# Kernel tuning notes

Hardware: AMD Instinct MI355X
Metric: run time of the kernel (lower is better)

Reference implementation:

```python
import jax, jax.numpy as jnp
import numpy as np

N_MEL = 80


def _bce_with_logits(x, t):
    # mean over all elements, numerically stable
    return jnp.mean(jnp.maximum(x, 0.0) - x * t + jnp.log1p(jnp.exp(-jnp.abs(x))))


def _spectral_mel_loss(pred, target):
    w = np.ones(N_MEL, dtype=np.float32)
    w[N_MEL // 4: 3 * N_MEL // 4] *= 1.5
    w[3 * N_MEL // 4:] *= 0.8
    w = jnp.asarray(w)[None, :, None]
    weighted_mse = jnp.mean((pred * w - target * w) ** 2)
    l1 = jnp.mean(jnp.abs(pred - target))
    dp = pred[:, :, 1:] - pred[:, :, :-1]
    dt = target[:, :, 1:] - target[:, :, :-1]
    spectral = jnp.mean((dp - dt) ** 2)
    return weighted_mse + 0.3 * l1 + 0.2 * spectral


def _perceptual_loss(pred, target):
    fw = jnp.exp(-jnp.arange(N_MEL, dtype=jnp.float32) / 20.0)[None, :, None]
    weighted = ((pred - target) ** 2) * fw
    l1 = jnp.mean(jnp.abs(pred - target))
    return jnp.mean(weighted) + 0.5 * l1


def _style_loss(pred, target):
    mean_loss = jnp.mean((jnp.mean(pred, axis=2) - jnp.mean(target, axis=2)) ** 2)
    # torch.var defaults to unbiased (ddof=1)
    var_loss = jnp.mean((jnp.var(pred, axis=2, ddof=1) - jnp.var(target, axis=2, ddof=1)) ** 2)
    c, t = pred.shape[1], pred.shape[2]
    gram_p = jnp.einsum('bct,bdt->bcd', pred, pred) / (c * t)
    gram_t = jnp.einsum('bct,bdt->bcd', target, target) / (c * t)
    gram_loss = jnp.mean((gram_p - gram_t) ** 2)
    return mean_loss + var_loss + 0.5 * gram_loss


def _monotonic_loss(att):
    # att: [B, mel_len, text_len]; vectorized form of the per-step violation loop
    b, mel_len, _ = att.shape
    peaks = jnp.argmax(att, axis=2).astype(jnp.float32)  # [B, mel_len]
    viol = jnp.maximum(peaks[:, :-1] - peaks[:, 1:], 0.0)
    return jnp.sum(viol) / (b * mel_len)


def setup_inputs() -> dict:
    key = jax.random.key(0)
    ks = jax.random.split(key, 6)
    B, C, T, L = 64, N_MEL, 2000, 200
    return {
        'mel_out': jax.random.normal(ks[0], (B, C, T), jnp.float32),
        'mel_out_postnet': jax.random.normal(ks[1], (B, C, T), jnp.float32),
        'mel_target': jax.random.normal(ks[2], (B, C, T), jnp.float32),
        'gate_out': jax.random.normal(ks[3], (B, T), jnp.float32),
        'gate_target': jax.random.uniform(ks[4], (B, T), jnp.float32),
        'attention_weights': jax.random.uniform(ks[5], (B, T, L), jnp.float32),
    }


def reference(mel_out, mel_out_postnet, mel_target, gate_out, gate_target, attention_weights):
    # loss weights (hparams defaults); guide_loss omitted (method truncated in source)
    mel_w, gate_w, spec_w, perc_w, style_w, mono_w = 1.0, 1.0, 0.3, 0.2, 0.1, 0.1
    gate_inner_w = 1.3  # AdaptiveGateLoss initial_weight

    mel_loss = jnp.mean((mel_out - mel_target) ** 2) + jnp.mean((mel_out_postnet - mel_target) ** 2)
    gate_loss = gate_inner_w * _bce_with_logits(gate_out.reshape(-1, 1), gate_target.reshape(-1, 1))
    spectral = _spectral_mel_loss(mel_out_postnet, mel_target)
    perceptual = _perceptual_loss(mel_out_postnet, mel_target)
    style = _style_loss(mel_out_postnet, mel_target)
    mono = _monotonic_loss(attention_weights)

    total = (mel_w * mel_loss + gate_w * gate_loss + spec_w * spectral
             + perc_w * perceptual + style_w * style + mono_w * mono)
    return total
```

## Files before the change

kernel.cpp:

```cpp
#include <hip/hip_runtime.h>
#include <math.h>

#define N_MEL 80
#define B_    64
#define T_    2000
#define L_    200
#define ROWS   (B_*N_MEL)
#define NTOT   (B_*N_MEL*T_)
#define GATE_N (B_*T_)
#define ATT_ROWS (B_*T_)
#define AV_ROWS 64
#define NVIOL  (ATT_ROWS/AV_ROWS)

#define G_ARGV   NVIOL
#define G_GATE   64
#define G_MELROW ROWS

#define WS_ROWPART 0
#define WS_M8      (WS_ROWPART + ROWS*8)
#define WS_GATEP   (WS_M8 + 8*64*6400)
#define WS_VIOLP   (WS_GATEP + 64)
#define WS_GFP     (WS_VIOLP + NVIOL)

typedef __attribute__((ext_vector_type(8)))  short bf16x8;
typedef __attribute__((ext_vector_type(16))) float f32x16;
typedef unsigned short ush;

__device__ __forceinline__ float blockReduceSum256(float v) {
    __shared__ float red[4];
    #pragma unroll
    for (int off = 32; off; off >>= 1) v += __shfl_down(v, off, 64);
    int lane = threadIdx.x & 63, w = threadIdx.x >> 6;
    if (lane == 0) red[w] = v;
    __syncthreads();
    if (threadIdx.x == 0) v = red[0] + red[1] + red[2] + red[3];
    return v;
}

__device__ __forceinline__ unsigned short f2bf(float f) {
    unsigned u = __float_as_uint(f);
    u = (u + 0x7fffu + ((u >> 16) & 1u)) >> 16;
    return (unsigned short)u;
}

__device__ __forceinline__ void scan_sub(const float* __restrict__ rowp, int q,
                                         float& bOut, int& pOut) {
    const float4* rp = (const float4*)rowp;
    float bx=-1.f, by=-1.f, bz=-1.f, bw=-1.f;
    int jx=0, jy=0, jz=0, jw=0;
    const int n = (q < 2) ? 13 : 12;
    #pragma unroll
    for (int i = 0; i < 13; i++) {
        if (i < n) {
            int j = q + 4*i;
            float4 v = rp[j];
            if (v.x > bx) { bx = v.x; jx = j; }
            if (v.y > by) { by = v.y; jy = j; }
            if (v.z > bz) { bz = v.z; jz = j; }
            if (v.w > bw) { bw = v.w; jw = j; }
        }
    }
    float b = bx; int p = 4*jx;
    if (by > b || (by == b && 4*jy+1 < p)) { b = by; p = 4*jy+1; }
    if (bz > b || (bz == b && 4*jz+2 < p)) { b = bz; p = 4*jz+2; }
    if (bw > b || (bw == b && 4*jw+3 < p)) { b = bw; p = 4*jw+3; }
    bOut = b; pOut = p;
}

__device__ __forceinline__ void merge4(float& b, int& p) {
    #pragma unroll
    for (int m = 1; m <= 2; m <<= 1) {
        float ob = __shfl_xor(b, m, 64);
        int   op = __shfl_xor(p, m, 64);
        if (ob > b || (ob == b && op < p)) { b = ob; p = op; }
    }
}

__global__ __launch_bounds__(256) void k_stream(const float* __restrict__ mo,
                                                const float* __restrict__ mp,
                                                const float* __restrict__ mt,
                                                const float* __restrict__ gx,
                                                const float* __restrict__ gt,
                                                const float* __restrict__ att,
                                                float* __restrict__ ws) {
    const int bid = blockIdx.x;
    float* rowpart = ws + WS_ROWPART;
    float* gatep   = ws + WS_GATEP;
    float* violp   = ws + WS_VIOLP;

    if (bid < G_ARGV) {
        __shared__ float pk[AV_ROWS + 1];
        const int ab = bid;
        const int g = threadIdx.x >> 2;
        const int q = threadIdx.x & 3;
        const int r0 = ab * AV_ROWS;
        const int r  = r0 + g;

        float b; int p;
        scan_sub(att + (long)r * L_, q, b, p);
        merge4(b, p);
        if (q == 0) pk[g] = (float)p;

        const int rb = r0 + AV_ROWS;
        const bool need_b = ((rb % T_) != 0) && (rb < ATT_ROWS);
        if (g == 0 && need_b) {
            float b2; int p2;
            scan_sub(att + (long)rb * L_, q, b2, p2);
            merge4(b2, p2);
            if (q == 0) pk[AV_ROWS] = (float)p2;
        }
        __syncthreads();

        float s = 0;
        if (threadIdx.x < AV_ROWS) {
            int rr = r0 + threadIdx.x;
            if (((rr + 1) % T_) != 0)
                s = fmaxf(pk[threadIdx.x] - pk[threadIdx.x + 1], 0.0f);
        }
        float tot = blockReduceSum256(s);
        if (threadIdx.x == 0) violp[ab] = tot;
        return;
    }

    if (bid < G_ARGV + G_GATE) {
        const int gb = bid - G_ARGV;
        const float4* x4 = (const float4*)gx;
        const float4* t4 = (const float4*)gt;
        float s = 0;
        for (int i = gb*256 + threadIdx.x; i < GATE_N/4; i += G_GATE*256) {
            float4 x = x4[i], t = t4[i];
            float xs[4] = {x.x, x.y, x.z, x.w}, ts[4] = {t.x, t.y, t.z, t.w};
            #pragma unroll
            for (int k = 0; k < 4; k++)
                s += fmaxf(xs[k], 0.0f) - xs[k]*ts[k] + log1pf(expf(-fabsf(xs[k])));
        }
        float tot = blockReduceSum256(s);
        if (threadIdx.x == 0) gatep[gb] = tot;
        return;
    }

    {
        const int row = bid - (G_ARGV + G_GATE);
        const long base = (long)row * T_;
        const float4* mo4 = (const float4*)(mo + base);
        const float4* mp4 = (const float4*)(mp + base);
        const float4* mt4 = (const float4*)(mt + base);

        float s1 = 0, s2 = 0, sl1 = 0, std_ = 0, sp = 0, sp2 = 0, st = 0, st2 = 0;
        for (int i = threadIdx.x; i < T_/4; i += 256) {
            float4 a = mo4[i], p = mp4[i], t = mt4[i];
            float e0 = a.x - t.x, e1 = a.y - t.y, e2 = a.z - t.z, e3 = a.w - t.w;
            s1 += e0*e0 + e1*e1 + e2*e2 + e3*e3;
            float d0 = p.x - t.x, d1 = p.y - t.y, d2 = p.z - t.z, d3 = p.w - t.w;
            s2 += d0*d0 + d1*d1 + d2*d2 + d3*d3;
            sl1 += fabsf(d0) + fabsf(d1) + fabsf(d2) + fabsf(d3);
            sp  += p.x + p.y + p.z + p.w;
            sp2 += p.x*p.x + p.y*p.y + p.z*p.z + p.w*p.w;
            st  += t.x + t.y + t.z + t.w;
            st2 += t.x*t.x + t.y*t.y + t.z*t.z + t.w*t.w;
            float q1 = d1 - d0, q2 = d2 - d1, q3 = d3 - d2;
            std_ += q1*q1 + q2*q2 + q3*q3;
            if (i > 0) {
                float dprev = mp[base + 4*i - 1] - mt[base + 4*i - 1];
                float q0 = d0 - dprev;
                std_ += q0*q0;
            }
        }

        __shared__ float red8[4][8];
        float vals[8] = {s1, s2, sl1, std_, sp, sp2, st, st2};
        #pragma unroll
        for (int k = 0; k < 8; k++) {
            float v = vals[k];
            #pragma unroll
            for (int off = 32; off; off >>= 1) v += __shfl_down(v, off, 64);
            vals[k] = v;
        }
        int lane = threadIdx.x & 63, w = threadIdx.x >> 6;
        if (lane == 0) {
            #pragma unroll
            for (int k = 0; k < 8; k++) red8[w][k] = vals[k];
        }
        __syncthreads();
        if (threadIdx.x == 0) {
            #pragma unroll
            for (int k = 0; k < 8; k++)
                rowpart[row*8 + k] = red8[0][k] + red8[1][k] + red8[2][k] + red8[3][k];
        }
    }
}

__global__ __launch_bounds__(192) void k_gram(const float* __restrict__ mp,
                                              const float* __restrict__ mt,
                                              float* __restrict__ M8) {
    const int b  = blockIdx.x >> 3;
    const int kc = blockIdx.x & 7;
    const int k0 = kc * 256;
    const int NS = (kc < 7) ? 16 : 13;

    __shared__ ush Dls[2][96][24];
    __shared__ ush Sls[2][96][24];

    const int tid  = threadIdx.x;
    const int row  = tid >> 1;
    const int half = tid & 1;
    const int lane = tid & 63;
    const int wv   = tid >> 6;
    const long bbase = (long)b * (N_MEL * T_);
    const float* prow = mp + bbase + (long)row * T_ + k0 + half * 8;
    const float* trow = mt + bbase + (long)row * T_ + k0 + half * 8;
    const bool rv = (row < N_MEL);

    f32x16 acc0 = {}, acc1 = {}, acc2 = {};
    float4 pa0, pa1, ta0, ta1;

    auto loadreg = [&](int s) {
        if (rv) {
            pa0 = *(const float4*)(prow + s*16);
            pa1 = *(const float4*)(prow + s*16 + 4);
            ta0 = *(const float4*)(trow + s*16);
            ta1 = *(const float4*)(trow + s*16 + 4);
        } else {
            pa0 = pa1 = ta0 = ta1 = make_float4(0.f, 0.f, 0.f, 0.f);
        }
    };
    auto writelds = [&](int buf) {
        bf16x8 d, s;
        d[0]=f2bf(pa0.x-ta0.x); d[1]=f2bf(pa0.y-ta0.y); d[2]=f2bf(pa0.z-ta0.z); d[3]=f2bf(pa0.w-ta0.w);
        d[4]=f2bf(pa1.x-ta1.x); d[5]=f2bf(pa1.y-ta1.y); d[6]=f2bf(pa1.z-ta1.z); d[7]=f2bf(pa1.w-ta1.w);
        s[0]=f2bf(pa0.x+ta0.x); s[1]=f2bf(pa0.y+ta0.y); s[2]=f2bf(pa0.z+ta0.z); s[3]=f2bf(pa0.w+ta0.w);
        s[4]=f2bf(pa1.x+ta1.x); s[5]=f2bf(pa1.y+ta1.y); s[6]=f2bf(pa1.z+ta1.z); s[7]=f2bf(pa1.w+ta1.w);
        *(bf16x8*)&Dls[buf][row][half*8] = d;
        *(bf16x8*)&Sls[buf][row][half*8] = s;
    };

    loadreg(0);
    writelds(0);
    __syncthreads();

    const int frow = lane & 31;
    const int fkh  = lane >> 5;
    for (int s = 0; s < NS; s++) {
        const int cur = s & 1;
        if (s + 1 < NS) loadreg(s + 1);
        bf16x8 af = *(const bf16x8*)&Dls[cur][wv*32 + frow][fkh*8];
        bf16x8 b0 = *(const bf16x8*)&Sls[cur][      frow][fkh*8];
        bf16x8 b1 = *(const bf16x8*)&Sls[cur][ 32 + frow][fkh*8];
        bf16x8 b2 = *(const bf16x8*)&Sls[cur][ 64 + frow][fkh*8];
        acc0 = __builtin_amdgcn_mfma_f32_32x32x16_bf16(af, b0, acc0, 0, 0, 0);
        acc1 = __builtin_amdgcn_mfma_f32_32x32x16_bf16(af, b1, acc1, 0, 0, 0);
        acc2 = __builtin_amdgcn_mfma_f32_32x32x16_bf16(af, b2, acc2, 0, 0, 0);
        if (s + 1 < NS) writelds((s + 1) & 1);
        __syncthreads();
    }

    float* Mb = M8 + ((long)(kc * B_ + b)) * 6400;
    #pragma unroll
    for (int r = 0; r < 16; r++) {
        int row32 = (r & 3) + 8 * (r >> 2) + 4 * (lane >> 5);
        int c = wv * 32 + row32;
        if (c < N_MEL) {
            Mb[c*80 + frow]      = acc0[r];
            Mb[c*80 + 32 + frow] = acc1[r];
            if (frow < 16) Mb[c*80 + 64 + frow] = acc2[r];
        }
    }
}

__global__ __launch_bounds__(256) void k_gramfin(const float* __restrict__ ws_ro,
                                                 float* __restrict__ gfp) {
    __shared__ float Ms[N_MEL][N_MEL + 1];
    const float* M8 = ws_ro + WS_M8;
    const int b = blockIdx.x;
    const float inv = 1.0f / (float)(N_MEL * T_);

    for (int i = threadIdx.x; i < 6400; i += 256) {
        float m = 0.f;
        #pragma unroll
        for (int kc = 0; kc < 8; kc++)
            m += M8[((long)(kc * B_ + b)) * 6400 + i];
        Ms[i / N_MEL][i % N_MEL] = m;
    }
    __syncthreads();

    float s = 0.f;
    for (int i = threadIdx.x; i < 6400; i += 256) {
        int c = i / N_MEL, d = i % N_MEL;
        float g = 0.5f * (Ms[c][d] + Ms[d][c]) * inv;
        s += g * g;
    }
    float tot = blockReduceSum256(s);
    if (threadIdx.x == 0) gfp[b] = tot;
}

__global__ __launch_bounds__(256) void k_final2(const float* __restrict__ ws_ro,
                                                float* __restrict__ out) {
    const float* rowpart = ws_ro + WS_ROWPART;
    const float* gatep   = ws_ro + WS_GATEP;
    const float* violp   = ws_ro + WS_VIOLP;
    const float* gfp     = ws_ro + WS_GFP;

    float a[11] = {0,0,0,0,0,0,0,0,0,0,0};
    for (int row = threadIdx.x; row < ROWS; row += 256) {
        const float4 lo = *(const float4*)(rowpart + row*8);
        const float4 hi = *(const float4*)(rowpart + row*8 + 4);
        int c = row % N_MEL;
        float wc = (c >= 3*N_MEL/4) ? 0.8f : ((c >= N_MEL/4) ? 1.5f : 1.0f);
        float fw = expf(-(float)c / 20.0f);
        a[0] += lo.x;
        a[1] += lo.y;
        a[2] += wc*wc*lo.y;
        a[3] += lo.z;
        a[4] += lo.w;
        a[5] += fw*lo.y;
        float md = (hi.x - hi.z) * (1.0f / T_);
        a[6] += md*md;
        float vp = (hi.y - hi.x*hi.x*(1.0f/T_)) * (1.0f/(T_-1));
        float vt = (hi.w - hi.z*hi.z*(1.0f/T_)) * (1.0f/(T_-1));
        float vd = vp - vt;
        a[7] += vd*vd;
    }
    for (int i = threadIdx.x; i < NVIOL; i += 256) a[9] += violp[i];
    if (threadIdx.x < 64) { a[8] = gatep[threadIdx.x]; a[10] = gfp[threadIdx.x]; }

    __shared__ float red[4][11];
    #pragma unroll
    for (int k = 0; k < 11; k++) {
        float v = a[k];
        #pragma unroll
        for (int off = 32; off; off >>= 1) v += __shfl_down(v, off, 64);
        a[k] = v;
    }
    int lane = threadIdx.x & 63, w = threadIdx.x >> 6;
    if (lane == 0) {
        #pragma unroll
        for (int k = 0; k < 11; k++) red[w][k] = a[k];
    }
    __syncthreads();
    if (threadIdx.x == 0) {
        float r[11];
        #pragma unroll
        for (int k = 0; k < 11; k++) r[k] = red[0][k] + red[1][k] + red[2][k] + red[3][k];
        const float invN = 1.0f / (float)NTOT;
        float mel        = (r[0] + r[1]) * invN;
        float gate       = 1.3f * r[8] / (float)GATE_N;
        float wmse       = r[2] * invN;
        float l1         = r[3] * invN;
        float sdiff      = r[4] / (float)(B_ * N_MEL * (T_ - 1));
        float spectral   = wmse + 0.3f*l1 + 0.2f*sdiff;
        float perceptual = r[5]*invN + 0.5f*l1;
        float mean_loss  = r[6] / (float)ROWS;
        float var_loss   = r[7] / (float)ROWS;
        float gram       = r[10] / (float)(B_ * 6400);
        float style      = mean_loss + var_loss + 0.5f*gram;
        float mono       = r[9] / (float)(B_ * T_);
        out[0] = mel + gate + 0.3f*spectral + 0.2f*perceptual + 0.1f*style + 0.1f*mono;
    }
}

extern "C" void kernel_launch(void* const* d_in, const int* in_sizes, int n_in,
                              void* d_out, int out_size, void* d_ws, size_t ws_size,
                              hipStream_t stream) {
    const float* mo  = (const float*)d_in[0];
    const float* mp  = (const float*)d_in[1];
    const float* mt  = (const float*)d_in[2];
    const float* gx  = (const float*)d_in[3];
    const float* gt  = (const float*)d_in[4];
    const float* att = (const float*)d_in[5];
    float* ws = (float*)d_ws;

    const int g1 = G_ARGV + G_GATE + G_MELROW;
    k_stream <<<g1,  256, 0, stream>>>(mo, mp, mt, gx, gt, att, ws);
    k_gram   <<<512, 192, 0, stream>>>(mp, mt, ws + WS_M8);
    k_gramfin<<<64,  256, 0, stream>>>(ws, ws + WS_GFP);
    k_final2 <<<1,   256, 0, stream>>>(ws, (float*)d_out);
}
```

Measured before the change: 90.60 us.

## Assign one wave per mel row with all loads issued up front

```diff
diff --git a/kernel.cpp b/kernel.cpp
--- a/kernel.cpp
+++ b/kernel.cpp
@@ -14,7 +14,7 @@
 
 #define G_ARGV   NVIOL
 #define G_GATE   64
-#define G_MELROW ROWS
+#define G_MELB   (ROWS/4)
 
 #define WS_ROWPART 0
 #define WS_M8      (WS_ROWPART + ROWS*8)
@@ -43,22 +43,32 @@
     return (unsigned short)u;
 }
 
+__device__ __forceinline__ void merge4(float& b, int& p) {
+    #pragma unroll
+    for (int m = 1; m <= 2; m <<= 1) {
+        float ob = __shfl_xor(b, m, 64);
+        int   op = __shfl_xor(p, m, 64);
+        if (ob > b || (ob == b && op < p)) { b = ob; p = op; }
+    }
+}
+
 __device__ __forceinline__ void scan_sub(const float* __restrict__ rowp, int q,
                                          float& bOut, int& pOut) {
     const float4* rp = (const float4*)rowp;
+    float4 v[13];
+    #pragma unroll
+    for (int i = 0; i < 12; i++) v[i] = rp[q + 4*i];
+    v[12] = make_float4(-1.f, -1.f, -1.f, -1.f);
+    if (q < 2) v[12] = rp[q + 48];
     float bx=-1.f, by=-1.f, bz=-1.f, bw=-1.f;
     int jx=0, jy=0, jz=0, jw=0;
-    const int n = (q < 2) ? 13 : 12;
     #pragma unroll
     for (int i = 0; i < 13; i++) {
-        if (i < n) {
-            int j = q + 4*i;
-            float4 v = rp[j];
-            if (v.x > bx) { bx = v.x; jx = j; }
-            if (v.y > by) { by = v.y; jy = j; }
-            if (v.z > bz) { bz = v.z; jz = j; }
-            if (v.w > bw) { bw = v.w; jw = j; }
-        }
+        int j = q + 4*i;
+        if (v[i].x > bx) { bx = v[i].x; jx = j; }
+        if (v[i].y > by) { by = v[i].y; jy = j; }
+        if (v[i].z > bz) { bz = v[i].z; jz = j; }
+        if (v[i].w > bw) { bw = v[i].w; jw = j; }
     }
     float b = bx; int p = 4*jx;
     if (by > b || (by == b && 4*jy+1 < p)) { b = by; p = 4*jy+1; }
@@ -67,22 +77,13 @@
     bOut = b; pOut = p;
 }
 
-__device__ __forceinline__ void merge4(float& b, int& p) {
-    #pragma unroll
-    for (int m = 1; m <= 2; m <<= 1) {
-        float ob = __shfl_xor(b, m, 64);
-        int   op = __shfl_xor(p, m, 64);
-        if (ob > b || (ob == b && op < p)) { b = ob; p = op; }
-    }
-}
-
-__global__ __launch_bounds__(256) void k_stream(const float* __restrict__ mo,
-                                                const float* __restrict__ mp,
-                                                const float* __restrict__ mt,
-                                                const float* __restrict__ gx,
-                                                const float* __restrict__ gt,
-                                                const float* __restrict__ att,
-                                                float* __restrict__ ws) {
+__global__ __launch_bounds__(256, 2) void k_stream(const float* __restrict__ mo,
+                                                   const float* __restrict__ mp,
+                                                   const float* __restrict__ mt,
+                                                   const float* __restrict__ gx,
+                                                   const float* __restrict__ gt,
+                                                   const float* __restrict__ att,
+                                                   float* __restrict__ ws) {
     const int bid = blockIdx.x;
     float* rowpart = ws + WS_ROWPART;
     float* gatep   = ws + WS_GATEP;
@@ -140,34 +141,52 @@
     }
 
     {
-        const int row = bid - (G_ARGV + G_GATE);
+        const int mb   = bid - (G_ARGV + G_GATE);
+        const int wid  = threadIdx.x >> 6;
+        const int lane = threadIdx.x & 63;
+        const int row  = mb * 4 + wid;
         const long base = (long)row * T_;
         const float4* mo4 = (const float4*)(mo + base);
         const float4* mp4 = (const float4*)(mp + base);
         const float4* mt4 = (const float4*)(mt + base);
 
-        float s1 = 0, s2 = 0, sl1 = 0, std_ = 0, sp = 0, sp2 = 0, st = 0, st2 = 0;
-        for (int i = threadIdx.x; i < T_/4; i += 256) {
-            float4 a = mo4[i], p = mp4[i], t = mt4[i];
-            float e0 = a.x - t.x, e1 = a.y - t.y, e2 = a.z - t.z, e3 = a.w - t.w;
+        float4 A[8], P[8], Q[8];
+        #pragma unroll
+        for (int k = 0; k < 7; k++) {
+            A[k] = mo4[lane + 64*k];
+            P[k] = mp4[lane + 64*k];
+            Q[k] = mt4[lane + 64*k];
+        }
+        const bool t7 = (lane < 52);
+        A[7] = make_float4(0.f,0.f,0.f,0.f);
+        P[7] = make_float4(0.f,0.f,0.f,0.f);
+        Q[7] = make_float4(0.f,0.f,0.f,0.f);
+        if (t7) { A[7] = mo4[lane + 448]; P[7] = mp4[lane + 448]; Q[7] = mt4[lane + 448]; }
+
+        float s1=0, s2=0, sl1=0, std_=0, sp=0, sp2=0, st=0, st2=0;
+        float carry = 0.f;
+        #pragma unroll
+        for (int k = 0; k < 8; k++) {
+            float4 a = A[k], p = P[k], t = Q[k];
+            float e0=a.x-t.x, e1=a.y-t.y, e2=a.z-t.z, e3=a.w-t.w;
             s1 += e0*e0 + e1*e1 + e2*e2 + e3*e3;
-            float d0 = p.x - t.x, d1 = p.y - t.y, d2 = p.z - t.z, d3 = p.w - t.w;
+            float d0=p.x-t.x, d1=p.y-t.y, d2=p.z-t.z, d3=p.w-t.w;
             s2 += d0*d0 + d1*d1 + d2*d2 + d3*d3;
             sl1 += fabsf(d0) + fabsf(d1) + fabsf(d2) + fabsf(d3);
             sp  += p.x + p.y + p.z + p.w;
             sp2 += p.x*p.x + p.y*p.y + p.z*p.z + p.w*p.w;
             st  += t.x + t.y + t.z + t.w;
             st2 += t.x*t.x + t.y*t.y + t.z*t.z + t.w*t.w;
-            float q1 = d1 - d0, q2 = d2 - d1, q3 = d3 - d2;
+            float q1 = d1-d0, q2 = d2-d1, q3 = d3-d2;
             std_ += q1*q1 + q2*q2 + q3*q3;
-            if (i > 0) {
-                float dprev = mp[base + 4*i - 1] - mt[base + 4*i - 1];
-                float q0 = d0 - dprev;
-                std_ += q0*q0;
-            }
-        }
-
-        __shared__ float red8[4][8];
+            float pv = __shfl_up(d3, 1, 64);
+            if (lane == 0) pv = carry;
+            float q0 = d0 - pv;
+            bool valid = !(k == 0 && lane == 0) && (k < 7 || t7);
+            if (valid) std_ += q0*q0;
+            carry = __shfl(d3, 63, 64);
+        }
+
         float vals[8] = {s1, s2, sl1, std_, sp, sp2, st, st2};
         #pragma unroll
         for (int k = 0; k < 8; k++) {
@@ -176,16 +195,9 @@
             for (int off = 32; off; off >>= 1) v += __shfl_down(v, off, 64);
             vals[k] = v;
         }
-        int lane = threadIdx.x & 63, w = threadIdx.x >> 6;
         if (lane == 0) {
-            #pragma unroll
-            for (int k = 0; k < 8; k++) red8[w][k] = vals[k];
-        }
-        __syncthreads();
-        if (threadIdx.x == 0) {
-            #pragma unroll
-            for (int k = 0; k < 8; k++)
-                rowpart[row*8 + k] = red8[0][k] + red8[1][k] + red8[2][k] + red8[3][k];
+            *(float4*)&rowpart[row*8]     = make_float4(vals[0], vals[1], vals[2], vals[3]);
+            *(float4*)&rowpart[row*8 + 4] = make_float4(vals[4], vals[5], vals[6], vals[7]);
         }
     }
 }
@@ -369,7 +381,7 @@
     const float* att = (const float*)d_in[5];
     float* ws = (float*)d_ws;
 
-    const int g1 = G_ARGV + G_GATE + G_MELROW;
+    const int g1 = G_ARGV + G_GATE + G_MELB;
     k_stream <<<g1,  256, 0, stream>>>(mo, mp, mt, gx, gt, att, ws);
     k_gram   <<<512, 192, 0, stream>>>(mp, mt, ws + WS_M8);
     k_gramfin<<<64,  256, 0, stream>>>(ws, ws + WS_GFP);
```

Measured after the change: 91.67 us. No clear change (+1.2%).

## Split fused stream kernel into separate mel-row and argmax/gate kernels

Applied to the files above, without the earlier changes.

```diff
diff --git a/kernel.cpp b/kernel.cpp
--- a/kernel.cpp
+++ b/kernel.cpp
@@ -12,10 +12,6 @@
 #define AV_ROWS 64
 #define NVIOL  (ATT_ROWS/AV_ROWS)
 
-#define G_ARGV   NVIOL
-#define G_GATE   64
-#define G_MELROW ROWS
-
 #define WS_ROWPART 0
 #define WS_M8      (WS_ROWPART + ROWS*8)
 #define WS_GATEP   (WS_M8 + 8*64*6400)
@@ -43,22 +39,32 @@
     return (unsigned short)u;
 }
 
+__device__ __forceinline__ void merge4(float& b, int& p) {
+    #pragma unroll
+    for (int m = 1; m <= 2; m <<= 1) {
+        float ob = __shfl_xor(b, m, 64);
+        int   op = __shfl_xor(p, m, 64);
+        if (ob > b || (ob == b && op < p)) { b = ob; p = op; }
+    }
+}
+
 __device__ __forceinline__ void scan_sub(const float* __restrict__ rowp, int q,
                                          float& bOut, int& pOut) {
     const float4* rp = (const float4*)rowp;
+    float4 v[13];
+    #pragma unroll
+    for (int i = 0; i < 12; i++) v[i] = rp[q + 4*i];
+    v[12] = make_float4(-1.f, -1.f, -1.f, -1.f);
+    if (q < 2) v[12] = rp[q + 48];
     float bx=-1.f, by=-1.f, bz=-1.f, bw=-1.f;
     int jx=0, jy=0, jz=0, jw=0;
-    const int n = (q < 2) ? 13 : 12;
     #pragma unroll
     for (int i = 0; i < 13; i++) {
-        if (i < n) {
-            int j = q + 4*i;
-            float4 v = rp[j];
-            if (v.x > bx) { bx = v.x; jx = j; }
-            if (v.y > by) { by = v.y; jy = j; }
-            if (v.z > bz) { bz = v.z; jz = j; }
-            if (v.w > bw) { bw = v.w; jw = j; }
-        }
+        int j = q + 4*i;
+        if (v[i].x > bx) { bx = v[i].x; jx = j; }
+        if (v[i].y > by) { by = v[i].y; jy = j; }
+        if (v[i].z > bz) { bz = v[i].z; jz = j; }
+        if (v[i].w > bw) { bw = v[i].w; jw = j; }
     }
     float b = bx; int p = 4*jx;
     if (by > b || (by == b && 4*jy+1 < p)) { b = by; p = 4*jy+1; }
@@ -67,126 +73,56 @@
     bOut = b; pOut = p;
 }
 
-__device__ __forceinline__ void merge4(float& b, int& p) {
-    #pragma unroll
-    for (int m = 1; m <= 2; m <<= 1) {
-        float ob = __shfl_xor(b, m, 64);
-        int   op = __shfl_xor(p, m, 64);
-        if (ob > b || (ob == b && op < p)) { b = ob; p = op; }
-    }
-}
-
-__global__ __launch_bounds__(256) void k_stream(const float* __restrict__ mo,
+__global__ __launch_bounds__(256) void k_melrow(const float* __restrict__ mo,
                                                 const float* __restrict__ mp,
                                                 const float* __restrict__ mt,
-                                                const float* __restrict__ gx,
-                                                const float* __restrict__ gt,
-                                                const float* __restrict__ att,
-                                                float* __restrict__ ws) {
-    const int bid = blockIdx.x;
-    float* rowpart = ws + WS_ROWPART;
-    float* gatep   = ws + WS_GATEP;
-    float* violp   = ws + WS_VIOLP;
-
-    if (bid < G_ARGV) {
-        __shared__ float pk[AV_ROWS + 1];
-        const int ab = bid;
-        const int g = threadIdx.x >> 2;
-        const int q = threadIdx.x & 3;
-        const int r0 = ab * AV_ROWS;
-        const int r  = r0 + g;
-
-        float b; int p;
-        scan_sub(att + (long)r * L_, q, b, p);
-        merge4(b, p);
-        if (q == 0) pk[g] = (float)p;
-
-        const int rb = r0 + AV_ROWS;
-        const bool need_b = ((rb % T_) != 0) && (rb < ATT_ROWS);
-        if (g == 0 && need_b) {
-            float b2; int p2;
-            scan_sub(att + (long)rb * L_, q, b2, p2);
-            merge4(b2, p2);
-            if (q == 0) pk[AV_ROWS] = (float)p2;
+                                                float* __restrict__ rowpart) {
+    const int row = blockIdx.x;
+    const long base = (long)row * T_;
+    const float4* mo4 = (const float4*)(mo + base);
+    const float4* mp4 = (const float4*)(mp + base);
+    const float4* mt4 = (const float4*)(mt + base);
+
+    float s1 = 0, s2 = 0, sl1 = 0, std_ = 0, sp = 0, sp2 = 0, st = 0, st2 = 0;
+    for (int i = threadIdx.x; i < T_/4; i += 256) {
+        float4 a = mo4[i], p = mp4[i], t = mt4[i];
+        float e0 = a.x - t.x, e1 = a.y - t.y, e2 = a.z - t.z, e3 = a.w - t.w;
+        s1 += e0*e0 + e1*e1 + e2*e2 + e3*e3;
+        float d0 = p.x - t.x, d1 = p.y - t.y, d2 = p.z - t.z, d3 = p.w - t.w;
+        s2 += d0*d0 + d1*d1 + d2*d2 + d3*d3;
+        sl1 += fabsf(d0) + fabsf(d1) + fabsf(d2) + fabsf(d3);
+        sp  += p.x + p.y + p.z + p.w;
+        sp2 += p.x*p.x + p.y*p.y + p.z*p.z + p.w*p.w;
+        st  += t.x + t.y + t.z + t.w;
+        st2 += t.x*t.x + t.y*t.y + t.z*t.z + t.w*t.w;
+        float q1 = d1 - d0, q2 = d2 - d1, q3 = d3 - d2;
+        std_ += q1*q1 + q2*q2 + q3*q3;
+        if (i > 0) {
+            float dprev = mp[base + 4*i - 1] - mt[base + 4*i - 1];
+            float q0 = d0 - dprev;
+            std_ += q0*q0;
         }
-        __syncthreads();
-
-        float s = 0;
-        if (threadIdx.x < AV_ROWS) {
-            int rr = r0 + threadIdx.x;
-            if (((rr + 1) % T_) != 0)
-                s = fmaxf(pk[threadIdx.x] - pk[threadIdx.x + 1], 0.0f);
-        }
-        float tot = blockReduceSum256(s);
-        if (threadIdx.x == 0) violp[ab] = tot;
-        return;
-    }
-
-    if (bid < G_ARGV + G_GATE) {
-        const int gb = bid - G_ARGV;
-        const float4* x4 = (const float4*)gx;
-        const float4* t4 = (const float4*)gt;
-        float s = 0;
-        for (int i = gb*256 + threadIdx.x; i < GATE_N/4; i += G_GATE*256) {
-            float4 x = x4[i], t = t4[i];
-            float xs[4] = {x.x, x.y, x.z, x.w}, ts[4] = {t.x, t.y, t.z, t.w};
-            #pragma unroll
-            for (int k = 0; k < 4; k++)
-                s += fmaxf(xs[k], 0.0f) - xs[k]*ts[k] + log1pf(expf(-fabsf(xs[k])));
-        }
-        float tot = blockReduceSum256(s);
-        if (threadIdx.x == 0) gatep[gb] = tot;
-        return;
-    }
-
-    {
-        const int row = bid - (G_ARGV + G_GATE);
-        const long base = (long)row * T_;
-        const float4* mo4 = (const float4*)(mo + base);
-        const float4* mp4 = (const float4*)(mp + base);
-        const float4* mt4 = (const float4*)(mt + base);
-
-        float s1 = 0, s2 = 0, sl1 = 0, std_ = 0, sp = 0, sp2 = 0, st = 0, st2 = 0;
-        for (int i = threadIdx.x; i < T_/4; i += 256) {
-            float4 a = mo4[i], p = mp4[i], t = mt4[i];
-            float e0 = a.x - t.x, e1 = a.y - t.y, e2 = a.z - t.z, e3 = a.w - t.w;
-            s1 += e0*e0 + e1*e1 + e2*e2 + e3*e3;
-            float d0 = p.x - t.x, d1 = p.y - t.y, d2 = p.z - t.z, d3 = p.w - t.w;
-            s2 += d0*d0 + d1*d1 + d2*d2 + d3*d3;
-            sl1 += fabsf(d0) + fabsf(d1) + fabsf(d2) + fabsf(d3);
-            sp  += p.x + p.y + p.z + p.w;
-            sp2 += p.x*p.x + p.y*p.y + p.z*p.z + p.w*p.w;
-            st  += t.x + t.y + t.z + t.w;
-            st2 += t.x*t.x + t.y*t.y + t.z*t.z + t.w*t.w;
-            float q1 = d1 - d0, q2 = d2 - d1, q3 = d3 - d2;
-            std_ += q1*q1 + q2*q2 + q3*q3;
-            if (i > 0) {
-                float dprev = mp[base + 4*i - 1] - mt[base + 4*i - 1];
-                float q0 = d0 - dprev;
-                std_ += q0*q0;
-            }
-        }
-
-        __shared__ float red8[4][8];
-        float vals[8] = {s1, s2, sl1, std_, sp, sp2, st, st2};
-        #pragma unroll
-        for (int k = 0; k < 8; k++) {
-            float v = vals[k];
-            #pragma unroll
-            for (int off = 32; off; off >>= 1) v += __shfl_down(v, off, 64);
-            vals[k] = v;
-        }
-        int lane = threadIdx.x & 63, w = threadIdx.x >> 6;
-        if (lane == 0) {
-            #pragma unroll
-            for (int k = 0; k < 8; k++) red8[w][k] = vals[k];
-        }
-        __syncthreads();
-        if (threadIdx.x == 0) {
-            #pragma unroll
-            for (int k = 0; k < 8; k++)
-                rowpart[row*8 + k] = red8[0][k] + red8[1][k] + red8[2][k] + red8[3][k];
-        }
+    }
+
+    __shared__ float red[4][8];
+    float vals[8] = {s1, s2, sl1, std_, sp, sp2, st, st2};
+    #pragma unroll
+    for (int k = 0; k < 8; k++) {
+        float v = vals[k];
+        #pragma unroll
+        for (int off = 32; off; off >>= 1) v += __shfl_down(v, off, 64);
+        vals[k] = v;
+    }
+    int lane = threadIdx.x & 63, w = threadIdx.x >> 6;
+    if (lane == 0) {
+        #pragma unroll
+        for (int k = 0; k < 8; k++) red[w][k] = vals[k];
+    }
+    __syncthreads();
+    if (threadIdx.x == 0) {
+        #pragma unroll
+        for (int k = 0; k < 8; k++)
+            rowpart[row*8 + k] = red[0][k] + red[1][k] + red[2][k] + red[3][k];
     }
 }
 
@@ -293,6 +229,62 @@
     if (threadIdx.x == 0) gfp[b] = tot;
 }
 
+__global__ __launch_bounds__(256, 2) void k_argviol(const float* __restrict__ att,
+                                                    const float* __restrict__ gx,
+                                                    const float* __restrict__ gt,
+                                                    float* __restrict__ ws) {
+    float* violp = ws + WS_VIOLP;
+    float* gatep = ws + WS_GATEP;
+
+    if (blockIdx.x >= NVIOL) {
+        const int gb = blockIdx.x - NVIOL;
+        const float4* x4 = (const float4*)gx;
+        const float4* t4 = (const float4*)gt;
+        float s = 0;
+        for (int i = gb*256 + threadIdx.x; i < GATE_N/4; i += 64*256) {
+            float4 x = x4[i], t = t4[i];
+            float xs[4] = {x.x, x.y, x.z, x.w}, ts[4] = {t.x, t.y, t.z, t.w};
+            #pragma unroll
+            for (int k = 0; k < 4; k++)
+                s += fmaxf(xs[k], 0.0f) - xs[k]*ts[k] + log1pf(expf(-fabsf(xs[k])));
+        }
+        float tot = blockReduceSum256(s);
+        if (threadIdx.x == 0) gatep[gb] = tot;
+        return;
+    }
+
+    __shared__ float pk[AV_ROWS + 1];
+    const int ab = blockIdx.x;
+    const int g = threadIdx.x >> 2;
+    const int q = threadIdx.x & 3;
+    const int r0 = ab * AV_ROWS;
+    const int r  = r0 + g;
+
+    float b; int p;
+    scan_sub(att + (long)r * L_, q, b, p);
+    merge4(b, p);
+    if (q == 0) pk[g] = (float)p;
+
+    const int rb = r0 + AV_ROWS;
+    const bool need_b = ((rb % T_) != 0) && (rb < ATT_ROWS);
+    if (g == 0 && need_b) {
+        float b2; int p2;
+        scan_sub(att + (long)rb * L_, q, b2, p2);
+        merge4(b2, p2);
+        if (q == 0) pk[AV_ROWS] = (float)p2;
+    }
+    __syncthreads();
+
+    float s = 0;
+    if (threadIdx.x < AV_ROWS) {
+        int rr = r0 + threadIdx.x;
+        if (((rr + 1) % T_) != 0)
+            s = fmaxf(pk[threadIdx.x] - pk[threadIdx.x + 1], 0.0f);
+    }
+    float tot = blockReduceSum256(s);
+    if (threadIdx.x == 0) violp[ab] = tot;
+}
+
 __global__ __launch_bounds__(256) void k_final2(const float* __restrict__ ws_ro,
                                                 float* __restrict__ out) {
     const float* rowpart = ws_ro + WS_ROWPART;
@@ -369,9 +361,9 @@
     const float* att = (const float*)d_in[5];
     float* ws = (float*)d_ws;
 
-    const int g1 = G_ARGV + G_GATE + G_MELROW;
-    k_stream <<<g1,  256, 0, stream>>>(mo, mp, mt, gx, gt, att, ws);
-    k_gram   <<<512, 192, 0, stream>>>(mp, mt, ws + WS_M8);
-    k_gramfin<<<64,  256, 0, stream>>>(ws, ws + WS_GFP);
-    k_final2 <<<1,   256, 0, stream>>>(ws, (float*)d_out);
-}
+    k_melrow <<<ROWS,       256, 0, stream>>>(mo, mp, mt, ws + WS_ROWPART);
+    k_gram   <<<512,        192, 0, stream>>>(mp, mt, ws + WS_M8);
+    k_gramfin<<<64,         256, 0, stream>>>(ws, ws + WS_GFP);
+    k_argviol<<<NVIOL + 64, 256, 0, stream>>>(att, gx, gt, ws);
+    k_final2 <<<1,          256, 0, stream>>>(ws, (float*)d_out);
+}
```

Result: slower. 93.62 us (+3.3%).
